# Kernel tuning notes

Measured on AMD Instinct MI355X. Metric: run time of the kernel, lower is better.

The kernel has to match this reference:

```python
import jax, jax.numpy as jnp
import numpy as np

N = 50000          # nodes
E_RAND = 800000    # random edges (avg degree 16)
IN, HID, HEADS, OUT = 256, 64, 4, 40
NEG_SLOPE = 0.2    # PyG GATConv default leaky_relu slope
BN_EPS = 1e-5


def setup_inputs() -> dict:
    key = jax.random.key(0)
    ks = jax.random.split(key, 24)
    x = jax.random.normal(ks[0], (N, IN), jnp.float32)
    ei = jax.random.randint(ks[1], (2, E_RAND), 0, N)
    loops = jnp.arange(N, dtype=ei.dtype)
    edge_index = jnp.concatenate([ei, jnp.stack([loops, loops])], axis=1)  # add self loops (PyG default)
    s = 0.1
    d = {
        "x": x,
        "edge_index": edge_index,
        "W0": jax.random.normal(ks[2], (IN, HEADS * HID), jnp.float32) * s,
        "a_src0": jax.random.normal(ks[3], (HEADS, HID), jnp.float32) * s,
        "a_dst0": jax.random.normal(ks[4], (HEADS, HID), jnp.float32) * s,
        "b0": jax.random.normal(ks[5], (HEADS * HID,), jnp.float32) * s,
        "bn0_g": jnp.ones((HEADS * HID,), jnp.float32),
        "bn0_b": jnp.zeros((HEADS * HID,), jnp.float32),
        "bn0_m": jax.random.normal(ks[6], (HEADS * HID,), jnp.float32) * s,
        "bn0_v": jax.random.uniform(ks[7], (HEADS * HID,), jnp.float32, 0.5, 1.5),
        "W1": jax.random.normal(ks[8], (HEADS * HID, HEADS * HID), jnp.float32) * s,
        "a_src1": jax.random.normal(ks[9], (HEADS, HID), jnp.float32) * s,
        "a_dst1": jax.random.normal(ks[10], (HEADS, HID), jnp.float32) * s,
        "b1": jax.random.normal(ks[11], (HEADS * HID,), jnp.float32) * s,
        "bn1_g": jnp.ones((HEADS * HID,), jnp.float32),
        "bn1_b": jnp.zeros((HEADS * HID,), jnp.float32),
        "bn1_m": jax.random.normal(ks[12], (HEADS * HID,), jnp.float32) * s,
        "bn1_v": jax.random.uniform(ks[13], (HEADS * HID,), jnp.float32, 0.5, 1.5),
        "W2": jax.random.normal(ks[14], (HEADS * HID, OUT), jnp.float32) * s,
        "a_src2": jax.random.normal(ks[15], (1, OUT), jnp.float32) * s,
        "a_dst2": jax.random.normal(ks[16], (1, OUT), jnp.float32) * s,
        "b2": jax.random.normal(ks[17], (OUT,), jnp.float32) * s,
    }
    return d


def gat_conv(x, edge_index, W, att_src, att_dst, heads, ch):
    """PyG GATConv (eval mode): gather -> leaky_relu attn -> segment softmax -> scatter add."""
    src, dst = edge_index[0], edge_index[1]
    h = (x @ W).reshape(-1, heads, ch)                       # [N,H,C]
    a_s = jnp.einsum('nhc,hc->nh', h, att_src)
    a_d = jnp.einsum('nhc,hc->nh', h, att_dst)
    e = jax.nn.leaky_relu(a_s[src] + a_d[dst], NEG_SLOPE)    # [E,H]
    m = jax.ops.segment_max(e, dst, num_segments=N)
    m = jax.lax.stop_gradient(jnp.where(jnp.isfinite(m), m, 0.0))
    p = jnp.exp(e - m[dst])
    denom = jax.ops.segment_sum(p, dst, num_segments=N)
    alpha = p / (denom[dst] + 1e-16)                         # [E,H]
    msg = h[src] * alpha[:, :, None]                         # [E,H,C]
    return jax.ops.segment_sum(msg, dst, num_segments=N)     # [N,H,C]


def _bn(h, g, b, m, v):
    return g * (h - m) * jax.lax.rsqrt(v + BN_EPS) + b


def reference(x, edge_index, W0, a_src0, a_dst0, b0, bn0_g, bn0_b, bn0_m, bn0_v,
              W1, a_src1, a_dst1, b1, bn1_g, bn1_b, bn1_m, bn1_v,
              W2, a_src2, a_dst2, b2):
    h = gat_conv(x, edge_index, W0, a_src0, a_dst0, HEADS, HID).reshape(N, HEADS * HID) + b0
    h = jax.nn.elu(_bn(h, bn0_g, bn0_b, bn0_m, bn0_v))
    h = gat_conv(h, edge_index, W1, a_src1, a_dst1, HEADS, HID).reshape(N, HEADS * HID) + b1
    h = jax.nn.elu(_bn(h, bn1_g, bn1_b, bn1_m, bn1_v))
    out = gat_conv(h, edge_index, W2, a_src2, a_dst2, 1, OUT).reshape(N, OUT) + b2
    return out
```

## Files before the change

### kernel.cpp

```cpp
#include <hip/hip_runtime.h>
#include <cstdint>
#include <cstddef>

constexpr int kN = 50000;
constexpr float kSlope = 0.2f;
constexpr float kBnEps = 1e-5f;

static inline int ceil_div(int a, int b) { return (a + b - 1) / b; }

typedef __attribute__((ext_vector_type(8))) short bf16x8;
typedef __attribute__((ext_vector_type(8))) unsigned short ushortx8;
typedef __attribute__((ext_vector_type(4))) float f32x4;

__device__ inline unsigned short f2bf(float f) {
  unsigned int u = __float_as_uint(f);
  u = (u + 0x7FFFu + ((u >> 16) & 1u)) >> 16;
  return (unsigned short)u;
}
__device__ inline float bf2f(unsigned short h) {
  return __uint_as_float(((unsigned int)h) << 16);
}


__global__ void k_degree(const int* __restrict__ dst, int* __restrict__ deg, int E) {
  int e = blockIdx.x * blockDim.x + threadIdx.x;
  if (e < E) atomicAdd(&deg[dst[e]], 1);
}

__global__ void k_scan1(const int* __restrict__ deg, int* __restrict__ rp,
                        int* __restrict__ bsum, int n) {
  __shared__ int sm[256];
  int i = blockIdx.x * 256 + threadIdx.x;
  int v = (i < n) ? deg[i] : 0;
  sm[threadIdx.x] = v;
  __syncthreads();
  for (int off = 1; off < 256; off <<= 1) {
    int t = (threadIdx.x >= off) ? sm[threadIdx.x - off] : 0;
    __syncthreads();
    sm[threadIdx.x] += t;
    __syncthreads();
  }
  if (i < n) rp[i + 1] = sm[threadIdx.x];
  if (threadIdx.x == 255) bsum[blockIdx.x] = sm[255];
}

__global__ void k_scan2(int* bsum, int nb) {
  __shared__ int sm[256];
  int v = (threadIdx.x < nb) ? bsum[threadIdx.x] : 0;
  sm[threadIdx.x] = v;
  __syncthreads();
  for (int off = 1; off < 256; off <<= 1) {
    int t = (threadIdx.x >= off) ? sm[threadIdx.x - off] : 0;
    __syncthreads();
    sm[threadIdx.x] += t;
    __syncthreads();
  }
  if (threadIdx.x < nb) bsum[threadIdx.x] = sm[threadIdx.x] - v;
}

__global__ void k_scan3(int* __restrict__ rp, const int* __restrict__ bsum, int n) {
  int i = blockIdx.x * 256 + threadIdx.x;
  if (i < n) rp[i + 1] += bsum[blockIdx.x];
  if (i == 0) rp[0] = 0;
}

__global__ void k_scatter(const int* __restrict__ src, const int* __restrict__ dst,
                          const int* __restrict__ rp, int* __restrict__ cur,
                          int* __restrict__ csr, int E) {
  int e = blockIdx.x * blockDim.x + threadIdx.x;
  if (e < E) {
    int d = dst[e];
    int pos = rp[d] + atomicAdd(&cur[d], 1);
    csr[pos] = src[e];
  }
}


__global__ void k_cast(const float* __restrict__ in, unsigned short* __restrict__ out, int n4) {
  int i = blockIdx.x * blockDim.x + threadIdx.x;
  if (i >= n4) return;
  float4 v = ((const float4*)in)[i];
  ushort4 o;
  o.x = f2bf(v.x);
  o.y = f2bf(v.y);
  o.z = f2bf(v.z);
  o.w = f2bf(v.w);
  ((ushort4*)out)[i] = o;
}

__global__ void k_transW3(const float* __restrict__ W0, unsigned short* __restrict__ Wt0,
                          const float* __restrict__ W1, unsigned short* __restrict__ Wt1,
                          const float* __restrict__ W2, unsigned short* __restrict__ Wt2) {
  int i = blockIdx.x * blockDim.x + threadIdx.x;
  const int S0 = 256 * 256, S1 = 256 * 256, S2 = 128 * 256;
  if (i < S0) {
    int nc = i >> 8, k = i & 255;
    Wt0[i] = f2bf(W0[(size_t)k * 256 + nc]);
  } else if (i < S0 + S1) {
    int j = i - S0;
    int nc = j >> 8, k = j & 255;
    Wt1[j] = f2bf(W1[(size_t)k * 256 + nc]);
  } else if (i < S0 + S1 + S2) {
    int j = i - S0 - S1;
    int nc = j >> 8, k = j & 255;
    Wt2[j] = (nc < 40) ? f2bf(W2[(size_t)k * 40 + nc]) : (unsigned short)0;
  }
}


__global__ __launch_bounds__(256) void k_mfma_gemm(const unsigned short* __restrict__ A,
                                                   const unsigned short* __restrict__ Bt,
                                                   unsigned short* __restrict__ C, int M, int K,
                                                   int Nc, int ldc) {
  constexpr int BM = 128, BK = 32, LDR = 40;
  __shared__ unsigned short As[BM * LDR];
  __shared__ unsigned short Bs[BM * LDR];
  int tid = threadIdx.x;
  int wave = tid >> 6, lane = tid & 63;
  int quad = lane >> 4, l16 = lane & 15;
  int wm = (wave & 1) * 64, wn = (wave >> 1) * 64;
  int bm = blockIdx.x * BM, bn = blockIdx.y * BM;
  f32x4 acc[4][4] = {};
  for (int k0 = 0; k0 < K; k0 += BK) {
#pragma unroll
    for (int it = 0; it < 2; it++) {
      int c = tid + it * 256;
      int row = c >> 2, part = c & 3;
      int gm = bm + row;
      ushortx8 va = (ushortx8)(0);
      if (gm < M) va = *(const ushortx8*)(A + (size_t)gm * K + k0 + part * 8);
      *(ushortx8*)(As + row * LDR + part * 8) = va;
      ushortx8 vb = *(const ushortx8*)(Bt + (size_t)(bn + row) * K + k0 + part * 8);
      *(ushortx8*)(Bs + row * LDR + part * 8) = vb;
    }
    __syncthreads();
    bf16x8 af[4], bf[4];
#pragma unroll
    for (int i = 0; i < 4; i++) {
      af[i] = *(const bf16x8*)(As + (wm + i * 16 + l16) * LDR + quad * 8);
      bf[i] = *(const bf16x8*)(Bs + (wn + i * 16 + l16) * LDR + quad * 8);
    }
#pragma unroll
    for (int i = 0; i < 4; i++)
#pragma unroll
      for (int j = 0; j < 4; j++)
        acc[i][j] = __builtin_amdgcn_mfma_f32_16x16x32_bf16(af[i], bf[j], acc[i][j], 0, 0, 0);
    __syncthreads();
  }
#pragma unroll
  for (int i = 0; i < 4; i++) {
#pragma unroll
    for (int j = 0; j < 4; j++) {
      int col = bn + wn + j * 16 + l16;
      if (col >= Nc) continue;
#pragma unroll
      for (int r = 0; r < 4; r++) {
        int row = bm + wm + i * 16 + quad * 4 + r;
        if (row < M) C[(size_t)row * ldc + col] = f2bf(acc[i][j][r]);
      }
    }
  }
}


__global__ __launch_bounds__(256) void k_attnproj_wave(const unsigned short* __restrict__ h,
                                                       const float* __restrict__ asrc,
                                                       const float* __restrict__ adst,
                                                       float* __restrict__ a_s,
                                                       float* __restrict__ a_d, int n_nodes) {
  int wid = (blockIdx.x * blockDim.x + threadIdx.x) >> 6;
  int lane = threadIdx.x & 63;
  if (wid >= n_nodes) return;
  int n = wid;
  int head = lane >> 4;
  int c = lane * 4;
  ushort4 hv = *(const ushort4*)(h + (size_t)n * 256 + c);
  float4 ws = *(const float4*)(asrc + c);
  float4 wd = *(const float4*)(adst + c);
  float v0 = bf2f(hv.x), v1 = bf2f(hv.y), v2 = bf2f(hv.z), v3 = bf2f(hv.w);
  float s = v0 * ws.x + v1 * ws.y + v2 * ws.z + v3 * ws.w;
  float d = v0 * wd.x + v1 * wd.y + v2 * wd.z + v3 * wd.w;
#pragma unroll
  for (int mask = 1; mask <= 8; mask <<= 1) {
    s += __shfl_xor(s, mask, 64);
    d += __shfl_xor(d, mask, 64);
  }
  if ((lane & 15) == 0) {
    a_s[n * 4 + head] = s;
    a_d[n * 4 + head] = d;
  }
}


__global__ void k_attnproj40(const unsigned short* __restrict__ h,
                             const float* __restrict__ asrc, const float* __restrict__ adst,
                             float* __restrict__ a_s, float* __restrict__ a_d, int n_nodes) {
  int n = blockIdx.x * blockDim.x + threadIdx.x;
  if (n >= n_nodes) return;
  const unsigned short* hp = h + (size_t)n * 64;
  float s = 0.f, d = 0.f;
  for (int c = 0; c < 40; c += 4) {
    ushort4 hv = *(const ushort4*)(hp + c);
    float4 wsv = *(const float4*)(asrc + c);
    float4 wdv = *(const float4*)(adst + c);
    float v0 = bf2f(hv.x), v1 = bf2f(hv.y), v2 = bf2f(hv.z), v3 = bf2f(hv.w);
    s += v0 * wsv.x + v1 * wsv.y + v2 * wsv.z + v3 * wsv.w;
    d += v0 * wdv.x + v1 * wdv.y + v2 * wdv.z + v3 * wdv.w;
  }
  a_s[n] = s;
  a_d[n] = d;
}


__global__ __launch_bounds__(256) void k_attn_agg256(
    const int* __restrict__ rp, const int* __restrict__ csr, const unsigned short* __restrict__ h,
    const float* __restrict__ a_s, const float* __restrict__ a_d, const float* __restrict__ bias,
    const float* __restrict__ bg, const float* __restrict__ bb, const float* __restrict__ bm,
    const float* __restrict__ bv, unsigned short* __restrict__ out, int n_nodes) {
  int wid = (blockIdx.x * blockDim.x + threadIdx.x) >> 6;
  int lane = threadIdx.x & 63;
  if (wid >= n_nodes) return;
  int n = wid;
  int beg = rp[n], end = rp[n + 1];
  int half = lane >> 5, l32 = lane & 31;
  int head = l32 >> 3;
  int c = l32 * 8;
  float ad = a_d[n * 4 + head];
  float acc[8] = {};
  float psum = 0.f;
  int e = beg;
  for (; e + 8 <= end; e += 8) {
    int s0 = csr[e + half];
    int s1 = csr[e + 2 + half];
    int s2 = csr[e + 4 + half];
    int s3 = csr[e + 6 + half];
    float x0 = a_s[s0 * 4 + head] + ad;
    float x1 = a_s[s1 * 4 + head] + ad;
    float x2 = a_s[s2 * 4 + head] + ad;
    float x3 = a_s[s3 * 4 + head] + ad;
    ushortx8 v0 = *(const ushortx8*)(h + (size_t)s0 * 256 + c);
    ushortx8 v1 = *(const ushortx8*)(h + (size_t)s1 * 256 + c);
    ushortx8 v2 = *(const ushortx8*)(h + (size_t)s2 * 256 + c);
    ushortx8 v3 = *(const ushortx8*)(h + (size_t)s3 * 256 + c);
    x0 = x0 > 0.f ? x0 : x0 * kSlope;
    x1 = x1 > 0.f ? x1 : x1 * kSlope;
    x2 = x2 > 0.f ? x2 : x2 * kSlope;
    x3 = x3 > 0.f ? x3 : x3 * kSlope;
    float p0 = __expf(x0), p1 = __expf(x1);
    float p2 = __expf(x2), p3 = __expf(x3);
    psum += (p0 + p1) + (p2 + p3);
#pragma unroll
    for (int j = 0; j < 8; j++) {
      acc[j] += bf2f(v0[j]) * p0 + bf2f(v1[j]) * p1;
      acc[j] += bf2f(v2[j]) * p2 + bf2f(v3[j]) * p3;
    }
  }
  for (; e + 2 <= end; e += 2) {
    int s0 = csr[e + half];
    float x0 = a_s[s0 * 4 + head] + ad;
    x0 = x0 > 0.f ? x0 : x0 * kSlope;
    float p0 = __expf(x0);
    psum += p0;
    ushortx8 v0 = *(const ushortx8*)(h + (size_t)s0 * 256 + c);
#pragma unroll
    for (int j = 0; j < 8; j++) acc[j] += bf2f(v0[j]) * p0;
  }
  if (e < end && half == 0) {
    int s0 = csr[e];
    float x0 = a_s[s0 * 4 + head] + ad;
    x0 = x0 > 0.f ? x0 : x0 * kSlope;
    float p0 = __expf(x0);
    psum += p0;
    ushortx8 v0 = *(const ushortx8*)(h + (size_t)s0 * 256 + c);
#pragma unroll
    for (int j = 0; j < 8; j++) acc[j] += bf2f(v0[j]) * p0;
  }
  psum += __shfl_xor(psum, 32, 64);
#pragma unroll
  for (int j = 0; j < 8; j++) acc[j] += __shfl_xor(acc[j], 32, 64);
  if (half == 0) {
    float rden = 1.f / (psum + 1e-16f);
    ushortx8 o;
#pragma unroll
    for (int j = 0; j < 8; j++) {
      float v = acc[j] * rden + bias[c + j];
      v = bg[c + j] * (v - bm[c + j]) * rsqrtf(bv[c + j] + kBnEps) + bb[c + j];
      v = v > 0.f ? v : (__expf(v) - 1.f);
      o[j] = f2bf(v);
    }
    *(ushortx8*)(out + (size_t)n * 256 + c) = o;
  }
}


__global__ __launch_bounds__(256) void k_attn_agg40(
    const int* __restrict__ rp, const int* __restrict__ csr, const unsigned short* __restrict__ h,
    const float* __restrict__ a_s, const float* __restrict__ a_d, const float* __restrict__ bias,
    float* __restrict__ out, int n_nodes) {
  int wid = (blockIdx.x * blockDim.x + threadIdx.x) >> 6;
  int lane = threadIdx.x & 63;
  if (wid >= n_nodes) return;
  int n = wid;
  int beg = rp[n], end = rp[n + 1];
  float ad = a_d[n];
  int grp = lane >> 3, l8 = lane & 7;
  int c = l8 * 8;
  float acc[8] = {};
  float psum = 0.f;
  for (int base = beg; base < end; base += 8) {
    int e = base + grp;
    if (e < end) {
      int s = csr[e];
      float x = a_s[s] + ad;
      x = x > 0.f ? x : x * kSlope;
      float p = __expf(x);
      psum += p;
      ushortx8 hv = *(const ushortx8*)(h + (size_t)s * 64 + c);
#pragma unroll
      for (int j = 0; j < 8; j++) acc[j] += bf2f(hv[j]) * p;
    }
  }
#pragma unroll
  for (int mask = 8; mask <= 32; mask <<= 1) psum += __shfl_xor(psum, mask, 64);
#pragma unroll
  for (int j = 0; j < 8; j++) {
#pragma unroll
    for (int mask = 8; mask <= 32; mask <<= 1) acc[j] += __shfl_xor(acc[j], mask, 64);
  }
  if (lane < 5) {
    float rden = 1.f / (psum + 1e-16f);
    float4 o0, o1;
    o0.x = acc[0] * rden + bias[c + 0];
    o0.y = acc[1] * rden + bias[c + 1];
    o0.z = acc[2] * rden + bias[c + 2];
    o0.w = acc[3] * rden + bias[c + 3];
    o1.x = acc[4] * rden + bias[c + 4];
    o1.y = acc[5] * rden + bias[c + 5];
    o1.z = acc[6] * rden + bias[c + 6];
    o1.w = acc[7] * rden + bias[c + 7];
    *(float4*)(out + (size_t)n * 40 + c) = o0;
    *(float4*)(out + (size_t)n * 40 + c + 4) = o1;
  }
}


extern "C" void kernel_launch(void* const* d_in, const int* in_sizes, int n_in, void* d_out,
                              int out_size, void* d_ws, size_t ws_size, hipStream_t stream) {
  const float* x = (const float*)d_in[0];
  const int* ei = (const int*)d_in[1];
  const float* W0 = (const float*)d_in[2];
  const float* as0 = (const float*)d_in[3];
  const float* ad0 = (const float*)d_in[4];
  const float* b0 = (const float*)d_in[5];
  const float* bg0 = (const float*)d_in[6];
  const float* bb0 = (const float*)d_in[7];
  const float* bm0 = (const float*)d_in[8];
  const float* bv0 = (const float*)d_in[9];
  const float* W1 = (const float*)d_in[10];
  const float* as1 = (const float*)d_in[11];
  const float* ad1 = (const float*)d_in[12];
  const float* b1 = (const float*)d_in[13];
  const float* bg1 = (const float*)d_in[14];
  const float* bb1 = (const float*)d_in[15];
  const float* bm1 = (const float*)d_in[16];
  const float* bv1 = (const float*)d_in[17];
  const float* W2 = (const float*)d_in[18];
  const float* as2 = (const float*)d_in[19];
  const float* ad2 = (const float*)d_in[20];
  const float* b2 = (const float*)d_in[21];
  float* out = (float*)d_out;

  const int E = in_sizes[1] / 2;
  const int* srcIdx = ei;
  const int* dstIdx = ei + E;

  char* p = (char*)d_ws;
  auto alloc = [&](size_t bytes) -> void* {
    void* r = (void*)p;
    p += (bytes + 255) & ~(size_t)255;
    return r;
  };
  int* rp = (int*)alloc((kN + 1) * sizeof(int));
  int* degcur = (int*)alloc((size_t)2 * kN * sizeof(int));
  int* deg = degcur;
  int* cur = degcur + kN;
  int* bsum = (int*)alloc(256 * sizeof(int));
  int* csr = (int*)alloc((size_t)E * sizeof(int));
  float* a_s = (float*)alloc((size_t)kN * 4 * sizeof(float));
  float* a_d = (float*)alloc((size_t)kN * 4 * sizeof(float));
  unsigned short* x16 = (unsigned short*)alloc((size_t)kN * 256 * 2);
  unsigned short* h16 = (unsigned short*)alloc((size_t)kN * 256 * 2);
  unsigned short* act16 = (unsigned short*)alloc((size_t)kN * 256 * 2);
  unsigned short* Wt0 = (unsigned short*)alloc((size_t)256 * 256 * 2);
  unsigned short* Wt1 = (unsigned short*)alloc((size_t)256 * 256 * 2);
  unsigned short* Wt2 = (unsigned short*)alloc((size_t)128 * 256 * 2);

  const int eb = ceil_div(E, 256);
  const int nb = ceil_div(kN, 256);

  hipMemsetAsync(degcur, 0, (size_t)2 * kN * sizeof(int), stream);
  k_degree<<<eb, 256, 0, stream>>>(dstIdx, deg, E);
  k_scan1<<<nb, 256, 0, stream>>>(deg, rp, bsum, kN);
  k_scan2<<<1, 256, 0, stream>>>(bsum, nb);
  k_scan3<<<nb, 256, 0, stream>>>(rp, bsum, kN);
  k_scatter<<<eb, 256, 0, stream>>>(srcIdx, dstIdx, rp, cur, csr, E);

  k_cast<<<ceil_div(kN * 64, 256), 256, 0, stream>>>(x, x16, kN * 64);
  k_transW3<<<ceil_div(256 * 256 * 2 + 128 * 256, 256), 256, 0, stream>>>(W0, Wt0, W1, Wt1, W2,
                                                                          Wt2);

  dim3 gg(ceil_div(kN, 128), 2);
  dim3 gg2(ceil_div(kN, 128), 1);
  int n1_blocks = ceil_div(kN, 256);
  int wpn_blocks = ceil_div(kN, 4);

  k_mfma_gemm<<<gg, 256, 0, stream>>>(x16, Wt0, h16, kN, 256, 256, 256);
  k_attnproj_wave<<<wpn_blocks, 256, 0, stream>>>(h16, as0, ad0, a_s, a_d, kN);
  k_attn_agg256<<<wpn_blocks, 256, 0, stream>>>(rp, csr, h16, a_s, a_d, b0, bg0, bb0, bm0, bv0,
                                                act16, kN);

  k_mfma_gemm<<<gg, 256, 0, stream>>>(act16, Wt1, h16, kN, 256, 256, 256);
  k_attnproj_wave<<<wpn_blocks, 256, 0, stream>>>(h16, as1, ad1, a_s, a_d, kN);
  k_attn_agg256<<<wpn_blocks, 256, 0, stream>>>(rp, csr, h16, a_s, a_d, b1, bg1, bb1, bm1, bv1,
                                                act16, kN);

  k_mfma_gemm<<<gg2, 256, 0, stream>>>(act16, Wt2, h16, kN, 256, 40, 64);
  k_attnproj40<<<n1_blocks, 256, 0, stream>>>(h16, as2, ad2, a_s, a_d, kN);
  k_attn_agg40<<<wpn_blocks, 256, 0, stream>>>(rp, csr, h16, a_s, a_d, b2, out, kN);
}
```

Baseline: 466.8 us.

## Fuse attention projections into GEMM epilogue and split aggregation across two waves

```diff
diff --git a/kernel.cpp b/kernel.cpp
--- a/kernel.cpp
+++ b/kernel.cpp
@@ -108,10 +108,11 @@
 }
 
 
-__global__ __launch_bounds__(256) void k_mfma_gemm(const unsigned short* __restrict__ A,
-                                                   const unsigned short* __restrict__ Bt,
-                                                   unsigned short* __restrict__ C, int M, int K,
-                                                   int Nc, int ldc) {
+__global__ __launch_bounds__(256) void k_mfma_gemm(
+    const unsigned short* __restrict__ A, const unsigned short* __restrict__ Bt,
+    unsigned short* __restrict__ C, const float* __restrict__ asrc,
+    const float* __restrict__ adst, float* __restrict__ a_s, float* __restrict__ a_d, int M,
+    int K, int Nc, int ldc, int heads, int acols) {
   constexpr int BM = 128, BK = 32, LDR = 40;
   __shared__ unsigned short As[BM * LDR];
   __shared__ unsigned short Bs[BM * LDR];
@@ -160,55 +161,39 @@
       }
     }
   }
-}
-
-
-__global__ __launch_bounds__(256) void k_attnproj_wave(const unsigned short* __restrict__ h,
-                                                       const float* __restrict__ asrc,
-                                                       const float* __restrict__ adst,
-                                                       float* __restrict__ a_s,
-                                                       float* __restrict__ a_d, int n_nodes) {
-  int wid = (blockIdx.x * blockDim.x + threadIdx.x) >> 6;
-  int lane = threadIdx.x & 63;
-  if (wid >= n_nodes) return;
-  int n = wid;
-  int head = lane >> 4;
-  int c = lane * 4;
-  ushort4 hv = *(const ushort4*)(h + (size_t)n * 256 + c);
-  float4 ws = *(const float4*)(asrc + c);
-  float4 wd = *(const float4*)(adst + c);
-  float v0 = bf2f(hv.x), v1 = bf2f(hv.y), v2 = bf2f(hv.z), v3 = bf2f(hv.w);
-  float s = v0 * ws.x + v1 * ws.y + v2 * ws.z + v3 * ws.w;
-  float d = v0 * wd.x + v1 * wd.y + v2 * wd.z + v3 * wd.w;
-#pragma unroll
-  for (int mask = 1; mask <= 8; mask <<= 1) {
-    s += __shfl_xor(s, mask, 64);
-    d += __shfl_xor(d, mask, 64);
-  }
-  if ((lane & 15) == 0) {
-    a_s[n * 4 + head] = s;
-    a_d[n * 4 + head] = d;
-  }
-}
-
-
-__global__ void k_attnproj40(const unsigned short* __restrict__ h,
-                             const float* __restrict__ asrc, const float* __restrict__ adst,
-                             float* __restrict__ a_s, float* __restrict__ a_d, int n_nodes) {
-  int n = blockIdx.x * blockDim.x + threadIdx.x;
-  if (n >= n_nodes) return;
-  const unsigned short* hp = h + (size_t)n * 64;
-  float s = 0.f, d = 0.f;
-  for (int c = 0; c < 40; c += 4) {
-    ushort4 hv = *(const ushort4*)(hp + c);
-    float4 wsv = *(const float4*)(asrc + c);
-    float4 wdv = *(const float4*)(adst + c);
-    float v0 = bf2f(hv.x), v1 = bf2f(hv.y), v2 = bf2f(hv.z), v3 = bf2f(hv.w);
-    s += v0 * wsv.x + v1 * wsv.y + v2 * wsv.z + v3 * wsv.w;
-    d += v0 * wdv.x + v1 * wdv.y + v2 * wdv.z + v3 * wdv.w;
-  }
-  a_s[n] = s;
-  a_d[n] = d;
+  int ghead = (bn + wn) >> 6;
+  if (ghead < heads) {
+    float asv[4], adv[4];
+#pragma unroll
+    for (int j = 0; j < 4; j++) {
+      int col = bn + wn + j * 16 + l16;
+      bool ok = col < acols;
+      asv[j] = ok ? asrc[col] : 0.f;
+      adv[j] = ok ? adst[col] : 0.f;
+    }
+#pragma unroll
+    for (int i = 0; i < 4; i++) {
+#pragma unroll
+      for (int r = 0; r < 4; r++) {
+        float s = acc[i][0][r] * asv[0] + acc[i][1][r] * asv[1] + acc[i][2][r] * asv[2] +
+                  acc[i][3][r] * asv[3];
+        float d = acc[i][0][r] * adv[0] + acc[i][1][r] * adv[1] + acc[i][2][r] * adv[2] +
+                  acc[i][3][r] * adv[3];
+#pragma unroll
+        for (int mask = 1; mask <= 8; mask <<= 1) {
+          s += __shfl_xor(s, mask, 64);
+          d += __shfl_xor(d, mask, 64);
+        }
+        if (l16 == 0) {
+          int row = bm + wm + i * 16 + quad * 4 + r;
+          if (row < M) {
+            a_s[row * heads + ghead] = s;
+            a_d[row * heads + ghead] = d;
+          }
+        }
+      }
+    }
+  }
 }
 
 
@@ -218,45 +203,35 @@
     const float* __restrict__ bg, const float* __restrict__ bb, const float* __restrict__ bm,
     const float* __restrict__ bv, unsigned short* __restrict__ out, int n_nodes) {
   int wid = (blockIdx.x * blockDim.x + threadIdx.x) >> 6;
+  int n = wid >> 1;
+  if (n >= n_nodes) return;
+  int chalf = (wid & 1) << 7;
   int lane = threadIdx.x & 63;
-  if (wid >= n_nodes) return;
-  int n = wid;
+  int q = lane >> 4, l16 = lane & 15;
+  int c = chalf + l16 * 8;
+  int head = c >> 6;
+  float ad = a_d[n * 4 + head];
   int beg = rp[n], end = rp[n + 1];
-  int half = lane >> 5, l32 = lane & 31;
-  int head = l32 >> 3;
-  int c = l32 * 8;
-  float ad = a_d[n * 4 + head];
   float acc[8] = {};
   float psum = 0.f;
   int e = beg;
   for (; e + 8 <= end; e += 8) {
-    int s0 = csr[e + half];
-    int s1 = csr[e + 2 + half];
-    int s2 = csr[e + 4 + half];
-    int s3 = csr[e + 6 + half];
+    int s0 = csr[e + q];
+    int s1 = csr[e + 4 + q];
     float x0 = a_s[s0 * 4 + head] + ad;
     float x1 = a_s[s1 * 4 + head] + ad;
-    float x2 = a_s[s2 * 4 + head] + ad;
-    float x3 = a_s[s3 * 4 + head] + ad;
     ushortx8 v0 = *(const ushortx8*)(h + (size_t)s0 * 256 + c);
     ushortx8 v1 = *(const ushortx8*)(h + (size_t)s1 * 256 + c);
-    ushortx8 v2 = *(const ushortx8*)(h + (size_t)s2 * 256 + c);
-    ushortx8 v3 = *(const ushortx8*)(h + (size_t)s3 * 256 + c);
     x0 = x0 > 0.f ? x0 : x0 * kSlope;
     x1 = x1 > 0.f ? x1 : x1 * kSlope;
-    x2 = x2 > 0.f ? x2 : x2 * kSlope;
-    x3 = x3 > 0.f ? x3 : x3 * kSlope;
     float p0 = __expf(x0), p1 = __expf(x1);
-    float p2 = __expf(x2), p3 = __expf(x3);
-    psum += (p0 + p1) + (p2 + p3);
-#pragma unroll
-    for (int j = 0; j < 8; j++) {
-      acc[j] += bf2f(v0[j]) * p0 + bf2f(v1[j]) * p1;
-      acc[j] += bf2f(v2[j]) * p2 + bf2f(v3[j]) * p3;
-    }
-  }
-  for (; e + 2 <= end; e += 2) {
-    int s0 = csr[e + half];
+    psum += p0 + p1;
+#pragma unroll
+    for (int j = 0; j < 8; j++) acc[j] += bf2f(v0[j]) * p0 + bf2f(v1[j]) * p1;
+  }
+  int rem = end - e;
+  if (q < rem) {
+    int s0 = csr[e + q];
     float x0 = a_s[s0 * 4 + head] + ad;
     x0 = x0 > 0.f ? x0 : x0 * kSlope;
     float p0 = __expf(x0);
@@ -265,20 +240,24 @@
 #pragma unroll
     for (int j = 0; j < 8; j++) acc[j] += bf2f(v0[j]) * p0;
   }
-  if (e < end && half == 0) {
-    int s0 = csr[e];
-    float x0 = a_s[s0 * 4 + head] + ad;
-    x0 = x0 > 0.f ? x0 : x0 * kSlope;
-    float p0 = __expf(x0);
-    psum += p0;
-    ushortx8 v0 = *(const ushortx8*)(h + (size_t)s0 * 256 + c);
-#pragma unroll
-    for (int j = 0; j < 8; j++) acc[j] += bf2f(v0[j]) * p0;
-  }
+  if (rem > 4 && q < rem - 4) {
+    int s1 = csr[e + 4 + q];
+    float x1 = a_s[s1 * 4 + head] + ad;
+    x1 = x1 > 0.f ? x1 : x1 * kSlope;
+    float p1 = __expf(x1);
+    psum += p1;
+    ushortx8 v1 = *(const ushortx8*)(h + (size_t)s1 * 256 + c);
+#pragma unroll
+    for (int j = 0; j < 8; j++) acc[j] += bf2f(v1[j]) * p1;
+  }
+  psum += __shfl_xor(psum, 16, 64);
   psum += __shfl_xor(psum, 32, 64);
 #pragma unroll
-  for (int j = 0; j < 8; j++) acc[j] += __shfl_xor(acc[j], 32, 64);
-  if (half == 0) {
+  for (int j = 0; j < 8; j++) {
+    acc[j] += __shfl_xor(acc[j], 16, 64);
+    acc[j] += __shfl_xor(acc[j], 32, 64);
+  }
+  if (q == 0) {
     float rden = 1.f / (psum + 1e-16f);
     ushortx8 o;
 #pragma unroll
@@ -307,10 +286,21 @@
   int c = l8 * 8;
   float acc[8] = {};
   float psum = 0.f;
-  for (int base = beg; base < end; base += 8) {
-    int e = base + grp;
-    if (e < end) {
-      int s = csr[e];
+  for (int base = beg; base < end; base += 16) {
+    int e0 = base + grp;
+    int e1 = base + 8 + grp;
+    if (e0 < end) {
+      int s = csr[e0];
+      float x = a_s[s] + ad;
+      x = x > 0.f ? x : x * kSlope;
+      float p = __expf(x);
+      psum += p;
+      ushortx8 hv = *(const ushortx8*)(h + (size_t)s * 64 + c);
+#pragma unroll
+      for (int j = 0; j < 8; j++) acc[j] += bf2f(hv[j]) * p;
+    }
+    if (e1 < end) {
+      int s = csr[e1];
       float x = a_s[s] + ad;
       x = x > 0.f ? x : x * kSlope;
       float p = __expf(x);
@@ -411,20 +401,20 @@
 
   dim3 gg(ceil_div(kN, 128), 2);
   dim3 gg2(ceil_div(kN, 128), 1);
-  int n1_blocks = ceil_div(kN, 256);
+  int agg256_blocks = ceil_div(2 * kN, 4);
   int wpn_blocks = ceil_div(kN, 4);
 
-  k_mfma_gemm<<<gg, 256, 0, stream>>>(x16, Wt0, h16, kN, 256, 256, 256);
-  k_attnproj_wave<<<wpn_blocks, 256, 0, stream>>>(h16, as0, ad0, a_s, a_d, kN);
-  k_attn_agg256<<<wpn_blocks, 256, 0, stream>>>(rp, csr, h16, a_s, a_d, b0, bg0, bb0, bm0, bv0,
-                                                act16, kN);
-
-  k_mfma_gemm<<<gg, 256, 0, stream>>>(act16, Wt1, h16, kN, 256, 256, 256);
-  k_attnproj_wave<<<wpn_blocks, 256, 0, stream>>>(h16, as1, ad1, a_s, a_d, kN);
-  k_attn_agg256<<<wpn_blocks, 256, 0, stream>>>(rp, csr, h16, a_s, a_d, b1, bg1, bb1, bm1, bv1,
-                                                act16, kN);
-
-  k_mfma_gemm<<<gg2, 256, 0, stream>>>(act16, Wt2, h16, kN, 256, 40, 64);
-  k_attnproj40<<<n1_blocks, 256, 0, stream>>>(h16, as2, ad2, a_s, a_d, kN);
+  k_mfma_gemm<<<gg, 256, 0, stream>>>(x16, Wt0, h16, as0, ad0, a_s, a_d, kN, 256, 256, 256, 4,
+                                      256);
+  k_attn_agg256<<<agg256_blocks, 256, 0, stream>>>(rp, csr, h16, a_s, a_d, b0, bg0, bb0, bm0,
+                                                   bv0, act16, kN);
+
+  k_mfma_gemm<<<gg, 256, 0, stream>>>(act16, Wt1, h16, as1, ad1, a_s, a_d, kN, 256, 256, 256, 4,
+                                      256);
+  k_attn_agg256<<<agg256_blocks, 256, 0, stream>>>(rp, csr, h16, a_s, a_d, b1, bg1, bb1, bm1,
+                                                   bv1, act16, kN);
+
+  k_mfma_gemm<<<gg2, 256, 0, stream>>>(act16, Wt2, h16, as2, ad2, a_s, a_d, kN, 256, 40, 64, 1,
+                                       40);
   k_attn_agg40<<<wpn_blocks, 256, 0, stream>>>(rp, csr, h16, a_s, a_d, b2, out, kN);
 }
```

Result: slower. 479.8 us (+2.8%).
